# Performance work log

Hardware: AMD Instinct MI355X
Metric: run time of the kernel (lower is better)

## Reference

```python
import jax, jax.numpy as jnp
import numpy as np

B, D, C = 4096, 256, 32000
T = 1.0
P_MARGIN = 0.5
N_MARGIN = 0.5
W_BU = 1.0
W_MS = 0.0
SIM_CAP = 0.999999


def setup_inputs() -> dict:
    key = jax.random.key(0)
    k1, k2, k3, k4, k5 = jax.random.split(key, 5)
    inputs = jax.random.normal(k1, (B, D), dtype=jnp.float32)
    inputs = inputs / jnp.linalg.norm(inputs, axis=1, keepdims=True)  # re-id features are L2-normalized
    targets = jax.random.randint(k2, (B,), 0, C, dtype=jnp.int32)
    indexs = jnp.arange(B, dtype=jnp.int32)
    label_to_pairs = jax.random.randint(k3, (B, 2), 0, B, dtype=jnp.int32)
    all_label_to_clusterid = jax.random.randint(k4, (C,), 0, C, dtype=jnp.int32)
    V = jax.random.normal(k5, (C, D), dtype=jnp.float32)
    V = V / jnp.linalg.norm(V, axis=1, keepdims=True)  # memory bank rows kept unit-norm by EMA update
    return {"inputs": inputs, "targets": targets, "indexs": indexs,
            "label_to_pairs": label_to_pairs,
            "all_label_to_clusterid": all_label_to_clusterid, "V": V}


def _ms_loss(inputs, targets):
    # vectorized form of ExLoss.ms with ms_table=False:
    # psims[i] = sims[i, targets==targets[i]], nsims[i] = sims[i, targets!=targets[i]]
    sims = inputs @ inputs.T  # [B, B]
    pos = targets[:, None] == targets[None, :]
    neg = ~pos
    NEG_BIG = jnp.float32(-1e30)
    POS_BIG = jnp.float32(1e30)
    p_thrd = jnp.where(neg.any(axis=1),
                       jnp.where(neg, sims, NEG_BIG).max(axis=1),
                       jnp.float32(-3.0)) + P_MARGIN
    n_thrd = jnp.where(pos.any(axis=1),
                       jnp.where(pos, sims, POS_BIG).min(axis=1),
                       jnp.float32(3.0)) - N_MARGIN
    hp = pos & (sims < p_thrd[:, None])
    hn = neg & (sims > n_thrd[:, None]) & (sims < SIM_CAP)
    hp_cnt = hp.sum()
    hn_cnt = hn.sum()
    # BCE-with-logits: target 1 -> softplus(-x); target 0 -> softplus(x); mean over kept elems
    hp_loss = jnp.where(hp_cnt > 0,
                        jnp.where(hp, jax.nn.softplus(-sims), 0.0).sum()
                        / jnp.maximum(hp_cnt, 1).astype(sims.dtype),
                        jnp.float32(0.0))
    hn_loss = jnp.where(hn_cnt > 0,
                        jnp.where(hn, jax.nn.softplus(sims), 0.0).sum()
                        / jnp.maximum(hn_cnt, 1).astype(sims.dtype),
                        jnp.float32(0.0))
    return hp_loss + hn_loss


def reference(inputs, targets, indexs, label_to_pairs, all_label_to_clusterid, V):
    # Exclusive.forward: logits against the memory bank
    tsims = inputs @ V.T            # [B, C]
    outputs = tsims * T
    # bu cross-entropy (weight=None, mean reduction)
    logp = jax.nn.log_softmax(outputs, axis=-1)
    bu_loss = -jnp.take_along_axis(logp, targets[:, None].astype(jnp.int32), axis=1).mean()
    ms_loss = _ms_loss(inputs, targets)
    loss = W_MS * ms_loss + W_BU * bu_loss
    return (loss, outputs)
```

## Files before the change

### kernel.cpp

```cpp
#include <hip/hip_runtime.h>
#include <hip/hip_bf16.h>
#include <stdint.h>

#define NB 4096
#define ND 256
#define NC 32000

typedef __bf16 bf16x8 __attribute__((ext_vector_type(8)));
typedef float  f32x4  __attribute__((ext_vector_type(4)));

__device__ __forceinline__ unsigned short f32_to_bf16(float f) {
  union { float f; uint32_t u; } v; v.f = f;
  uint32_t r = v.u + 0x7fffu + ((v.u >> 16) & 1u);
  return (unsigned short)(r >> 16);
}

__global__ void prep_kernel(const float* __restrict__ inA,
                            const float* __restrict__ inV,
                            unsigned short* __restrict__ outA,
                            unsigned short* __restrict__ outV,
                            float* __restrict__ rowsum,
                            float* __restrict__ loss) {
  int gid = blockIdx.x * blockDim.x + threadIdx.x;
  int stride = gridDim.x * blockDim.x;
  if (gid == 0) *loss = 0.f;
  for (int i = gid; i < NB; i += stride) rowsum[i] = 0.f;
  const int nA4 = NB * ND / 4;
  const int nV4 = NC * ND / 4;
  for (int i = gid; i < nA4 + nV4; i += stride) {
    float4 v = (i < nA4) ? ((const float4*)inA)[i]
                         : ((const float4*)inV)[i - nA4];
    ushort4 o;
    o.x = f32_to_bf16(v.x);
    o.y = f32_to_bf16(v.y);
    o.z = f32_to_bf16(v.z);
    o.w = f32_to_bf16(v.w);
    if (i < nA4) ((ushort4*)outA)[i] = o;
    else         ((ushort4*)outV)[i - nA4] = o;
  }
}

__global__ void __launch_bounds__(256, 2)
gemm_expsum_kernel(const unsigned short* __restrict__ A,
                   const unsigned short* __restrict__ V,
                   float* __restrict__ out,
                   float* __restrict__ rowsum) {
  __shared__ float tls[4][16][68];

  const int tid  = threadIdx.x;
  const int lane = tid & 63;
  const int wave = tid >> 6;
  const int wr   = wave >> 1;
  const int wc   = wave & 1;
  const int c16  = lane & 15;
  const int kq   = lane >> 4;

  const int brow = blockIdx.x * 128;
  const int bcol = blockIdx.y * 128;

  const __bf16* Ab = (const __bf16*)A;
  const __bf16* Vb = (const __bf16*)V;
  const __bf16* aBase = Ab + (size_t)(brow + wr * 64 + c16) * ND + kq * 8;
  const __bf16* bBase = Vb + (size_t)(bcol + wc * 64 + c16) * ND + kq * 8;

  f32x4 acc[4][4];
#pragma unroll
  for (int m = 0; m < 4; ++m)
#pragma unroll
    for (int n = 0; n < 4; ++n)
      acc[m][n] = (f32x4){0.f, 0.f, 0.f, 0.f};

  bf16x8 a0[4], b0[4], a1[4], b1[4];

#define LOADF(AF, BF, KT)                                                     \
  do {                                                                        \
    _Pragma("unroll")                                                         \
    for (int m = 0; m < 4; ++m)                                               \
      AF[m] = *(const bf16x8*)(aBase + (size_t)m * 16 * ND + (KT) * 32);      \
    _Pragma("unroll")                                                         \
    for (int n = 0; n < 4; ++n)                                               \
      BF[n] = *(const bf16x8*)(bBase + (size_t)n * 16 * ND + (KT) * 32);      \
  } while (0)

#define MFMAALL(AF, BF)                                                       \
  do {                                                                        \
    _Pragma("unroll")                                                         \
    for (int m = 0; m < 4; ++m)                                               \
      _Pragma("unroll")                                                       \
      for (int n = 0; n < 4; ++n)                                             \
        acc[m][n] = __builtin_amdgcn_mfma_f32_16x16x32_bf16(AF[m], BF[n],     \
                                                            acc[m][n], 0, 0, 0); \
  } while (0)

  LOADF(a0, b0, 0);
#pragma unroll
  for (int kt = 0; kt < 8; kt += 2) {
    if (kt + 1 < 8) LOADF(a1, b1, kt + 1);
    MFMAALL(a0, b0);
    if (kt + 2 < 8) LOADF(a0, b0, kt + 2);
    MFMAALL(a1, b1);
  }

#pragma unroll
  for (int m = 0; m < 4; ++m) {
#pragma unroll
    for (int n = 0; n < 4; ++n)
#pragma unroll
      for (int r = 0; r < 4; ++r)
        tls[wave][kq * 4 + r][n * 16 + c16] = acc[m][n][r];
    asm volatile("s_waitcnt lgkmcnt(0)" ::: "memory");
    __builtin_amdgcn_sched_barrier(0);
#pragma unroll
    for (int rr = 0; rr < 4; ++rr) {
      const int lr = rr * 4 + kq;
      float4 v = *(const float4*)&tls[wave][lr][c16 * 4];
      const int grow = brow + wr * 64 + m * 16 + lr;
      *(float4*)(out + (size_t)grow * NC + bcol + wc * 64 + c16 * 4) = v;
      float s = __expf(v.x) + __expf(v.y) + __expf(v.z) + __expf(v.w);
      s += __shfl_xor(s, 1);
      s += __shfl_xor(s, 2);
      s += __shfl_xor(s, 4);
      s += __shfl_xor(s, 8);
      if (c16 == 0) atomicAdd(&rowsum[grow], s);
    }
    asm volatile("s_waitcnt lgkmcnt(0)" ::: "memory");
    __builtin_amdgcn_sched_barrier(0);
  }
#undef LOADF
#undef MFMAALL
}

__global__ void finalize_kernel(const float* __restrict__ rowsum,
                                const float* __restrict__ out,
                                const int* __restrict__ targets,
                                float* __restrict__ loss) {
  int i = blockIdx.x * blockDim.x + threadIdx.x;
  float li = 0.f;
  if (i < NB) {
    float lse = logf(rowsum[i]);
    float xt  = out[(size_t)i * NC + targets[i]];
    li = lse - xt;
  }
#pragma unroll
  for (int o = 32; o > 0; o >>= 1) li += __shfl_down(li, o);
  __shared__ float wsum[4];
  int lane = threadIdx.x & 63, wv = threadIdx.x >> 6;
  if (lane == 0) wsum[wv] = li;
  __syncthreads();
  if (threadIdx.x == 0) {
    float s = wsum[0] + wsum[1] + wsum[2] + wsum[3];
    atomicAdd(loss, s * (1.0f / NB));
  }
}

extern "C" void kernel_launch(void* const* d_in, const int* in_sizes, int n_in,
                              void* d_out, int out_size, void* d_ws, size_t ws_size,
                              hipStream_t stream) {
  const float* inputs  = (const float*)d_in[0];
  const int*   targets = (const int*)d_in[1];
  const float* V       = (const float*)d_in[5];

  float* loss    = (float*)d_out;
  float* outputs = (float*)d_out + 1;

  char* ws = (char*)d_ws;
  unsigned short* Abf = (unsigned short*)ws;
  unsigned short* Vbf = (unsigned short*)(ws + (size_t)NB * ND * 2);
  float* rowsum = (float*)(ws + (size_t)NB * ND * 2 + (size_t)NC * ND * 2);

  hipLaunchKernelGGL(prep_kernel, dim3(2048), dim3(256), 0, stream,
                     inputs, V, Abf, Vbf, rowsum, loss);
  hipLaunchKernelGGL(gemm_expsum_kernel, dim3(NB / 128, NC / 128), dim3(256), 0, stream,
                     Abf, Vbf, outputs, rowsum);
  hipLaunchKernelGGL(finalize_kernel, dim3(NB / 256), dim3(256), 0, stream,
                     rowsum, outputs, targets, loss);
}
```

Baseline: 328.6 us.

## Swap MFMA operands for direct row stores and remap blocks per XCD

The MFMA operands are swapped (V fragment as A, inputs as B), so each lane's accumulator holds four consecutive output columns of one row. The epilogue can then store float4s straight from registers and reduce exp-sums with two shuffles, with no shared-memory transpose. The grid becomes a 1D launch remapped so each XCD owns a contiguous range of 32 column tiles, to improve L2 reuse of V rows. The remapping launches some idle blocks that exit early (8192 launched for 8000 tiles). Each 16-byte store now covers only part of a row, so write coalescing may be less efficient.

Result: slower. 348.4 us (+6.0%).

```diff
diff --git a/kernel.cpp b/kernel.cpp
--- a/kernel.cpp
+++ b/kernel.cpp
@@ -45,7 +45,14 @@
                    const unsigned short* __restrict__ V,
                    float* __restrict__ out,
                    float* __restrict__ rowsum) {
-  __shared__ float tls[4][16][68];
+  const int b = blockIdx.x;
+  const int xcd = b & 7;
+  const int s = b >> 3;
+  const int colt = (xcd << 5) + (s & 31);
+  const int rowt = s >> 5;
+  if (colt >= NC / 128) return;
+  const int brow = rowt << 7;
+  const int bcol = colt << 7;
 
   const int tid  = threadIdx.x;
   const int lane = tid & 63;
@@ -55,9 +62,6 @@
   const int c16  = lane & 15;
   const int kq   = lane >> 4;
 
-  const int brow = blockIdx.x * 128;
-  const int bcol = blockIdx.y * 128;
-
   const __bf16* Ab = (const __bf16*)A;
   const __bf16* Vb = (const __bf16*)V;
   const __bf16* aBase = Ab + (size_t)(brow + wr * 64 + c16) * ND + kq * 8;
@@ -65,10 +69,10 @@
 
   f32x4 acc[4][4];
 #pragma unroll
-  for (int m = 0; m < 4; ++m)
+  for (int c = 0; c < 4; ++c)
 #pragma unroll
-    for (int n = 0; n < 4; ++n)
-      acc[m][n] = (f32x4){0.f, 0.f, 0.f, 0.f};
+    for (int r = 0; r < 4; ++r)
+      acc[c][r] = (f32x4){0.f, 0.f, 0.f, 0.f};
 
   bf16x8 a0[4], b0[4], a1[4], b1[4];
 
@@ -85,11 +89,11 @@
 #define MFMAALL(AF, BF)                                                       \
   do {                                                                        \
     _Pragma("unroll")                                                         \
-    for (int m = 0; m < 4; ++m)                                               \
+    for (int c = 0; c < 4; ++c)                                               \
       _Pragma("unroll")                                                       \
-      for (int n = 0; n < 4; ++n)                                             \
-        acc[m][n] = __builtin_amdgcn_mfma_f32_16x16x32_bf16(AF[m], BF[n],     \
-                                                            acc[m][n], 0, 0, 0); \
+      for (int r = 0; r < 4; ++r)                                             \
+        acc[c][r] = __builtin_amdgcn_mfma_f32_16x16x32_bf16(BF[c], AF[r],     \
+                                                            acc[c][r], 0, 0, 0); \
   } while (0)
 
   LOADF(a0, b0, 0);
@@ -102,29 +106,19 @@
   }
 
 #pragma unroll
-  for (int m = 0; m < 4; ++m) {
+  for (int r = 0; r < 4; ++r) {
+    const int grow = brow + wr * 64 + r * 16 + c16;
+    float* prow = out + (size_t)grow * NC + (bcol + wc * 64 + kq * 4);
+    float sum = 0.f;
 #pragma unroll
-    for (int n = 0; n < 4; ++n)
-#pragma unroll
-      for (int r = 0; r < 4; ++r)
-        tls[wave][kq * 4 + r][n * 16 + c16] = acc[m][n][r];
-    asm volatile("s_waitcnt lgkmcnt(0)" ::: "memory");
-    __builtin_amdgcn_sched_barrier(0);
-#pragma unroll
-    for (int rr = 0; rr < 4; ++rr) {
-      const int lr = rr * 4 + kq;
-      float4 v = *(const float4*)&tls[wave][lr][c16 * 4];
-      const int grow = brow + wr * 64 + m * 16 + lr;
-      *(float4*)(out + (size_t)grow * NC + bcol + wc * 64 + c16 * 4) = v;
-      float s = __expf(v.x) + __expf(v.y) + __expf(v.z) + __expf(v.w);
-      s += __shfl_xor(s, 1);
-      s += __shfl_xor(s, 2);
-      s += __shfl_xor(s, 4);
-      s += __shfl_xor(s, 8);
-      if (c16 == 0) atomicAdd(&rowsum[grow], s);
+    for (int c = 0; c < 4; ++c) {
+      f32x4 v = acc[c][r];
+      *(f32x4*)(prow + c * 16) = v;
+      sum += __expf(v[0]) + __expf(v[1]) + __expf(v[2]) + __expf(v[3]);
     }
-    asm volatile("s_waitcnt lgkmcnt(0)" ::: "memory");
-    __builtin_amdgcn_sched_barrier(0);
+    sum += __shfl_xor(sum, 16);
+    sum += __shfl_xor(sum, 32);
+    if (lane < 16) atomicAdd(&rowsum[grow], sum);
   }
 #undef LOADF
 #undef MFMAALL
@@ -170,7 +164,7 @@
 
   hipLaunchKernelGGL(prep_kernel, dim3(2048), dim3(256), 0, stream,
                      inputs, V, Abf, Vbf, rowsum, loss);
-  hipLaunchKernelGGL(gemm_expsum_kernel, dim3(NB / 128, NC / 128), dim3(256), 0, stream,
+  hipLaunchKernelGGL(gemm_expsum_kernel, dim3(8 * 1024), dim3(256), 0, stream,
                      Abf, Vbf, outputs, rowsum);
   hipLaunchKernelGGL(finalize_kernel, dim3(NB / 256), dim3(256), 0, stream,
                      rowsum, outputs, targets, loss);
```
